# Optimization experiments

Measured on AMD Instinct MI355X. Metric: run time of the kernel, lower is better.

Reference implementation:

```python
import jax, jax.numpy as jnp
import numpy as np

H = 8          # head_num
DK = 16        # qkv_dim
CLIP = 10.0    # logit clipping


def _heads(x):
    # (b, n, H*DK) -> (b, H, n, DK)
    b, n, _ = x.shape
    return x.reshape(b, n, H, DK).transpose(0, 2, 1, 3)


def setup_inputs() -> dict:
    key = jax.random.key(0)
    ks = jax.random.split(key, 10)
    batch, problem, d, klen = 2048, 100, 128, 10
    s = 1.0 / np.sqrt(d)
    problems = jax.random.uniform(ks[0], (batch, problem, 2), dtype=jnp.float32)
    encoded_nodes = jax.random.normal(ks[1], (batch, problem, d), dtype=jnp.float32)
    Wq_first = jax.random.normal(ks[2], (d, H * DK), dtype=jnp.float32) * s
    Wq_last = jax.random.normal(ks[3], (d, H * DK), dtype=jnp.float32) * s
    Wk = jax.random.normal(ks[4], (d, H * DK), dtype=jnp.float32) * s
    Wv = jax.random.normal(ks[5], (d, H * DK), dtype=jnp.float32) * s
    Wcomb = jax.random.normal(ks[6], (H * DK, d), dtype=jnp.float32) * s
    # prefix: k distinct node indices per batch row (first k of a random permutation)
    perm = jax.vmap(lambda kk: jax.random.permutation(kk, problem))(
        jax.random.split(ks[7], batch))
    prefix = perm[:, :klen].astype(jnp.int32)
    return {"problems": problems, "encoded_nodes": encoded_nodes,
            "Wq_first": Wq_first, "Wq_last": Wq_last, "Wk": Wk, "Wv": Wv,
            "Wcomb": Wcomb, "prefix": prefix}


def reference(problems, encoded_nodes, Wq_first, Wq_last, Wk, Wv, Wcomb, prefix):
    batch, problem, d = encoded_nodes.shape
    b_idx = jnp.arange(batch)
    sqrt_dk = jnp.sqrt(jnp.float32(DK))
    sqrt_d = jnp.sqrt(jnp.float32(d))

    # set_kv: precompute multi-head K, V once (single-head key = encoded_nodes)
    kh = _heads(encoded_nodes @ Wk)   # (b, H, n, DK)
    vh = _heads(encoded_nodes @ Wv)   # (b, H, n, DK)

    # set_q1: query contribution of the first node (last node of prefix)
    last0 = prefix[:, -1]
    q1 = _heads(encoded_nodes[b_idx, last0][:, None, :] @ Wq_first)  # (b, H, 1, DK)

    # visited mask from prefix
    visited0 = jnp.zeros((batch, problem), dtype=bool)
    visited0 = visited0.at[b_idx[:, None], prefix].set(True)

    def step(carry, _):
        visited, cur = carry
        enc_last = encoded_nodes[b_idx, cur][:, None, :]            # (b, 1, d)
        q = q1 + _heads(enc_last @ Wq_last)                         # (b, H, 1, DK)
        ninf = jnp.where(visited, -jnp.inf, 0.0)                    # (b, n)
        scores = jnp.einsum('bhqe,bhne->bhqn', q, kh) / sqrt_dk
        att = jax.nn.softmax(scores + ninf[:, None, None, :], axis=-1)
        mh = jnp.einsum('bhqn,bhne->bhqe', att, vh)                 # (b, H, 1, DK)
        mh = mh.transpose(0, 2, 1, 3).reshape(batch, 1, H * DK) @ Wcomb  # (b, 1, d)
        sc = jnp.einsum('bqd,bnd->bqn', mh, encoded_nodes)[:, 0] / sqrt_d  # (b, n)
        logits = CLIP * jnp.tanh(sc) + ninf
        sel = jnp.argmax(logits, axis=-1)                           # (b,)
        visited = visited.at[b_idx, sel].set(True)
        return (visited, sel), sel

    steps = problem - prefix.shape[1]
    _, sels = jax.lax.scan(step, (visited0, last0), None, length=steps)
    tour = jnp.concatenate([prefix, sels.T.astype(prefix.dtype)], axis=1)  # (b, problem)
    return tour
```

## Files before the change

### kernel.cpp

```cpp
#include <hip/hip_runtime.h>
#include <math.h>

#define N      100
#define D      128
#define KL     10
#define S0     90
#define STEPS  90
#define LDK    132
#define NT     512

__device__ __forceinline__ float dot4(float4 a, float4 b) {
  return a.x*b.x + a.y*b.y + a.z*b.z + a.w*b.w;
}
__device__ __forceinline__ void fma4(float4& acc, float a, float4 v) {
  acc.x += a*v.x; acc.y += a*v.y; acc.z += a*v.z; acc.w += a*v.w;
}

template<int RPT>
__device__ __forceinline__ void cc(const float* __restrict__ encB,
                                   const float* __restrict__ W,
                                   bool wRowMajor, int base, int cnt,
                                   const int* __restrict__ slotNode,
                                   float* __restrict__ stage, int tid) {
  const int col = tid & 127;
  const int grp = tid >> 7;
  float acc[RPT];
  int   nd [RPT];
  #pragma unroll
  for (int ii = 0; ii < RPT; ++ii) {
    acc[ii] = 0.f;
    int r = grp + 4*ii;
    nd[ii] = (r < cnt) ? __builtin_amdgcn_readfirstlane(slotNode[base + r]) : 0;
  }
  for (int dd = 0; dd < D; dd += 16) {
    float w[16];
    #pragma unroll
    for (int t = 0; t < 16; ++t)
      w[t] = wRowMajor ? W[col*D + dd + t] : W[(dd+t)*D + col];
    #pragma unroll
    for (int ii = 0; ii < RPT; ++ii) {
      int r = grp + 4*ii;
      if (r < cnt) {
        const float* er = encB + (size_t)nd[ii]*D + dd;
        float a0=0,a1=0,a2=0,a3=0;
        #pragma unroll
        for (int t = 0; t < 16; t += 4) {
          a0 += er[t]*w[t];   a1 += er[t+1]*w[t+1];
          a2 += er[t+2]*w[t+2]; a3 += er[t+3]*w[t+3];
        }
        acc[ii] += (a0+a1)+(a2+a3);
      }
    }
  }
  #pragma unroll
  for (int ii = 0; ii < RPT; ++ii) {
    int r = grp + 4*ii;
    if (r < cnt) stage[(base + r)*LDK + col] = acc[ii];
  }
}

__global__ __launch_bounds__(NT, 4)
void policy_kernel(const float* __restrict__ enc,
                   const float* __restrict__ Wq_first,
                   const float* __restrict__ Wq_last,
                   const float* __restrict__ Wk,
                   const float* __restrict__ Wv,
                   const float* __restrict__ Wcomb,
                   const int*   __restrict__ prefix,
                   int*         __restrict__ out) {
  __shared__ __align__(16) float sCE[S0*LDK];
  __shared__ __align__(16) float sq[D];
  __shared__ __align__(16) float sMh[D];
  __shared__ int   sSlotNode[96];
  __shared__ unsigned long long sPacked[2];
  __shared__ int   sLast0;

  const int tid = threadIdx.x;
  const int b   = blockIdx.x;
  const float* encB = enc + (size_t)b*N*D;

  if (tid < KL) out[(size_t)b*N + tid] = prefix[b*KL + tid];
  if (tid == 0) {
    unsigned vis[4] = {0u,0u,0u,0u};
    const int* pr = prefix + b*KL;
    for (int j = 0; j < KL; ++j) { int n = pr[j]; vis[n>>5] |= 1u << (n&31); }
    int cnt = 0;
    for (int n = 0; n < N; ++n)
      if (!((vis[n>>5] >> (n&31)) & 1u)) sSlotNode[cnt++] = n;
    sLast0 = pr[KL-1];
    sPacked[0] = 0ull; sPacked[1] = 0ull;
  }
  __syncthreads();

  if (tid < D) {
    const int last0 = sLast0;
    const float* er = encB + (size_t)last0*D;
    float a0=0,a1=0,a2=0,a3=0;
    #pragma unroll
    for (int d = 0; d < D; d += 4) {
      a0 += er[d]  *Wq_first[d*D     + tid];
      a1 += er[d+1]*Wq_first[(d+1)*D + tid];
      a2 += er[d+2]*Wq_first[(d+2)*D + tid];
      a3 += er[d+3]*Wq_first[(d+3)*D + tid];
    }
    sMh[tid] = (a0+a1)+(a2+a3);
  }
  __syncthreads();

  const int h = tid >> 6, l = tid & 63;

  {
    const int col = tid & 127;
    const int grp = tid >> 7;
    float acc[23]; int nd[23];
    #pragma unroll
    for (int ii = 0; ii < 23; ++ii) {
      int r = grp + 4*ii;
      acc[ii] = 0.f;
      nd[ii] = (r < S0) ? __builtin_amdgcn_readfirstlane(sSlotNode[r])
                        : ((r == S0) ? sLast0 : 0);
    }
    for (int dd = 0; dd < D; dd += 16) {
      float w[16];
      #pragma unroll
      for (int t = 0; t < 16; ++t) w[t] = Wq_last[(dd+t)*D + col];
      #pragma unroll
      for (int ii = 0; ii < 23; ++ii) {
        int r = grp + 4*ii;
        if (r <= S0) {
          const float* er = encB + (size_t)nd[ii]*D + dd;
          float a0=0,a1=0,a2=0,a3=0;
          #pragma unroll
          for (int t = 0; t < 16; t += 4) {
            a0 += er[t]*w[t];   a1 += er[t+1]*w[t+1];
            a2 += er[t+2]*w[t+2]; a3 += er[t+3]*w[t+3];
          }
          acc[ii] += (a0+a1)+(a2+a3);
        }
      }
    }
    #pragma unroll
    for (int ii = 0; ii < 23; ++ii) {
      int r = grp + 4*ii;
      if (r < S0)       sCE[r*LDK + col] = acc[ii];
      else if (r == S0) sq[col] = acc[ii] + sMh[col];
    }
  }
  __syncthreads();

  const int qcol = (h << 4) | (l & 15);
  const int qrg  = l >> 4;
  float qp[23];
  {
    const float q1c = sMh[qcol];
    #pragma unroll
    for (int ii = 0; ii < 23; ++ii) {
      int r = qrg + 4*ii;
      qp[ii] = (r < S0) ? (sCE[r*LDK + qcol] + q1c) : 0.f;
    }
  }
  __syncthreads();

  cc<23>(encB, Wk, false, 0, S0, sSlotNode, sCE, tid);
  __syncthreads();
  float4 ka0,ka1,ka2,ka3, kb0,kb1,kb2,kb3;
  {
    const float* p = &sCE[l*LDK + h*16];
    ka0 = *(const float4*)(p+0);  ka1 = *(const float4*)(p+4);
    ka2 = *(const float4*)(p+8);  ka3 = *(const float4*)(p+12);
  }
  if (l < 26) {
    const float* p = &sCE[(64+l)*LDK + h*16];
    kb0 = *(const float4*)(p+0);  kb1 = *(const float4*)(p+4);
    kb2 = *(const float4*)(p+8);  kb3 = *(const float4*)(p+12);
  } else {
    kb0=kb1=kb2=kb3 = make_float4(0.f,0.f,0.f,0.f);
  }
  __syncthreads();

  const int cQuad = tid >> 4;
  const int cStrm = tid & 15;
  cc<12>(encB, Wv, false,  0, 48, sSlotNode, sCE, tid);
  cc<12>(encB, Wv, false, 48, 42, sSlotNode, sCE, tid);
  __syncthreads();
  float4 v0,v1,v2,v3,v4,v5;
  v0 = *(const float4*)&sCE[(cStrm     )*LDK + cQuad*4];
  v1 = *(const float4*)&sCE[(cStrm + 16)*LDK + cQuad*4];
  v2 = *(const float4*)&sCE[(cStrm + 32)*LDK + cQuad*4];
  v3 = *(const float4*)&sCE[(cStrm + 48)*LDK + cQuad*4];
  v4 = *(const float4*)&sCE[(cStrm + 64)*LDK + cQuad*4];
  v5 = (cStrm < 10) ? *(const float4*)&sCE[(cStrm + 80)*LDK + cQuad*4]
                    : make_float4(0.f,0.f,0.f,0.f);
  __syncthreads();

  cc<6>(encB, Wcomb, true,  0, 24, sSlotNode, sCE, tid);
  cc<6>(encB, Wcomb, true, 24, 24, sSlotNode, sCE, tid);
  cc<6>(encB, Wcomb, true, 48, 24, sSlotNode, sCE, tid);
  cc<6>(encB, Wcomb, true, 72, 18, sSlotNode, sCE, tid);
  __syncthreads();

  const int di  = tid >> 2;
  const int dkc = tid & 3;
  float visA = 0.f, visB = 0.f, visD = 0.f;

  for (int step = 0; step < STEPS; ++step) {
    float x0, x1;
    {
      const float4 q0 = *(const float4*)&sq[h*16 + 0];
      const float4 q1 = *(const float4*)&sq[h*16 + 4];
      const float4 q2 = *(const float4*)&sq[h*16 + 8];
      const float4 q3 = *(const float4*)&sq[h*16 + 12];
      float s0 = dot4(q0,ka0)+dot4(q1,ka1)+dot4(q2,ka2)+dot4(q3,ka3);
      x0 = expf(s0*0.25f + visA);
      x1 = 0.f;
      if (l < 26) {
        float s1 = dot4(q0,kb0)+dot4(q1,kb1)+dot4(q2,kb2)+dot4(q3,kb3);
        x1 = expf(s1*0.25f + visB);
      }
    }

    {
      const float a0 = __shfl(x0, cStrm);
      const float a1 = __shfl(x0, cStrm + 16);
      const float a2 = __shfl(x0, cStrm + 32);
      const float a3 = __shfl(x0, cStrm + 48);
      const float a4 = __shfl(x1, cStrm);
      const float a5 = __shfl(x1, cStrm + 16);
      float s_loc = (a0+a1)+(a2+a3)+(a4+a5);
      float4 acc = make_float4(0.f,0.f,0.f,0.f);
      fma4(acc, a0, v0);
      fma4(acc, a1, v1);
      fma4(acc, a2, v2);
      fma4(acc, a3, v3);
      fma4(acc, a4, v4);
      fma4(acc, a5, v5);
      #pragma unroll
      for (int off = 1; off < 16; off <<= 1) {
        acc.x += __shfl_xor(acc.x, off);
        acc.y += __shfl_xor(acc.y, off);
        acc.z += __shfl_xor(acc.z, off);
        acc.w += __shfl_xor(acc.w, off);
        s_loc += __shfl_xor(s_loc, off);
      }
      if (cStrm == 0) {
        const float r = 1.0f / s_loc;
        float4 o; o.x=acc.x*r; o.y=acc.y*r; o.z=acc.z*r; o.w=acc.w*r;
        *(float4*)&sMh[((cQuad & 7) << 4) + ((cQuad >> 3) << 2)] = o;
      }
    }
    __syncthreads();

    if (tid == NT-1) sPacked[(step+1)&1] = 0ull;

    if (tid < 384) {
      float a = 0.f;
      #pragma unroll
      for (int j = 0; j < 8; ++j) {
        const float4 ce = *(const float4*)&sCE[di*LDK + dkc*32 + j*4];
        const float4 mh = *(const float4*)&sMh[j*16 + dkc*4];
        a += dot4(ce, mh);
      }
      a += __shfl_xor(a, 1);
      a += __shfl_xor(a, 2);
      float val = (di < S0) ? a + visD : -INFINITY;
      int   idx = (di < S0) ? di : 127;
      #pragma unroll
      for (int off = 4; off <= 32; off <<= 1) {
        float ov = __shfl_xor(val, off);
        int   oi = __shfl_xor(idx, off);
        if (ov > val || (ov == val && oi < idx)) { val = ov; idx = oi; }
      }
      if (l == 0) {
        unsigned s = __float_as_uint(val);
        s = (s & 0x80000000u) ? ~s : (s | 0x80000000u);
        unsigned long long pk = ((unsigned long long)s << 32)
                              | (unsigned long long)(unsigned)(127 - idx);
        atomicMax(&sPacked[step&1], pk);
      }
    }
    __syncthreads();

    {
      const unsigned long long u = sPacked[step & 1];
      const int idx = __builtin_amdgcn_readfirstlane(127 - (int)(u & 0xFFull));
      if (tid == 0) out[(size_t)b*N + KL + step] = sSlotNode[idx];
      if (idx == l)      visA = -INFINITY;
      if (idx == l + 64) visB = -INFINITY;
      if (idx == di)     visD = -INFINITY;
      const int want = idx >> 2;
      float qv = qp[0];
      #pragma unroll
      for (int ii = 1; ii < 23; ++ii) qv = (want == ii) ? qp[ii] : qv;
      if (qrg == (idx & 3)) sq[qcol] = qv;
    }
  }
}

extern "C" void kernel_launch(void* const* d_in, const int* in_sizes, int n_in,
                              void* d_out, int out_size, void* d_ws, size_t ws_size,
                              hipStream_t stream) {
  const float* enc      = (const float*)d_in[1];
  const float* Wq_first = (const float*)d_in[2];
  const float* Wq_last  = (const float*)d_in[3];
  const float* Wk       = (const float*)d_in[4];
  const float* Wv       = (const float*)d_in[5];
  const float* Wcomb    = (const float*)d_in[6];
  const int*   prefix   = (const int*)d_in[7];
  const int batch = in_sizes[7] / KL;
  policy_kernel<<<batch, NT, 0, stream>>>(enc, Wq_first, Wq_last, Wk, Wv, Wcomb,
                                          prefix, (int*)d_out);
}
```

Baseline: 2.280 ms.

## Keep per-node queries in shared memory and hold combined-encoding rows in registers

Moves the Wq_last projection to the end of setup and stores all 91 query rows (bias q1 added) in a shared table. Each step indexes that table by the current node instead of selecting from 23 per-thread registers and writing sq. The Wcomb-projected encoding rows used for the logits are loaded once into 32 registers per thread, so the step loop no longer reads them from shared memory. This trades more register pressure under launch_bounds(512,4) for fewer shared loads and a simpler per-step update.

```diff
diff --git a/kernel.cpp b/kernel.cpp
--- a/kernel.cpp
+++ b/kernel.cpp
@@ -59,6 +59,50 @@
   }
 }
 
+template<int RPT>
+__device__ __forceinline__ void ccq(const float* __restrict__ encB,
+                                    const float* __restrict__ W,
+                                    int base, int cnt,
+                                    const int* __restrict__ slotNode,
+                                    const float* __restrict__ bias,
+                                    float* __restrict__ stage, int tid) {
+  const int col = tid & 127;
+  const int grp = tid >> 7;
+  float acc[RPT];
+  int   nd [RPT];
+  #pragma unroll
+  for (int ii = 0; ii < RPT; ++ii) {
+    acc[ii] = 0.f;
+    int r = grp + 4*ii;
+    nd[ii] = (r < cnt) ? __builtin_amdgcn_readfirstlane(slotNode[base + r]) : 0;
+  }
+  for (int dd = 0; dd < D; dd += 16) {
+    float w[16];
+    #pragma unroll
+    for (int t = 0; t < 16; ++t) w[t] = W[(dd+t)*D + col];
+    #pragma unroll
+    for (int ii = 0; ii < RPT; ++ii) {
+      int r = grp + 4*ii;
+      if (r < cnt) {
+        const float* er = encB + (size_t)nd[ii]*D + dd;
+        float a0=0,a1=0,a2=0,a3=0;
+        #pragma unroll
+        for (int t = 0; t < 16; t += 4) {
+          a0 += er[t]*w[t];   a1 += er[t+1]*w[t+1];
+          a2 += er[t+2]*w[t+2]; a3 += er[t+3]*w[t+3];
+        }
+        acc[ii] += (a0+a1)+(a2+a3);
+      }
+    }
+  }
+  const float bq = bias[col];
+  #pragma unroll
+  for (int ii = 0; ii < RPT; ++ii) {
+    int r = grp + 4*ii;
+    if (r < cnt) stage[(base + r)*LDK + col] = acc[ii] + bq;
+  }
+}
+
 __global__ __launch_bounds__(NT, 4)
 void policy_kernel(const float* __restrict__ enc,
                    const float* __restrict__ Wq_first,
@@ -68,8 +112,7 @@
                    const float* __restrict__ Wcomb,
                    const int*   __restrict__ prefix,
                    int*         __restrict__ out) {
-  __shared__ __align__(16) float sCE[S0*LDK];
-  __shared__ __align__(16) float sq[D];
+  __shared__ __align__(16) float sQ[(S0+1)*LDK];
   __shared__ __align__(16) float sMh[D];
   __shared__ int   sSlotNode[96];
   __shared__ unsigned long long sPacked[2];
@@ -88,6 +131,7 @@
     for (int n = 0; n < N; ++n)
       if (!((vis[n>>5] >> (n&31)) & 1u)) sSlotNode[cnt++] = n;
     sLast0 = pr[KL-1];
+    sSlotNode[S0] = pr[KL-1];
     sPacked[0] = 0ull; sPacked[1] = 0ull;
   }
   __syncthreads();
@@ -109,68 +153,16 @@
 
   const int h = tid >> 6, l = tid & 63;
 
-  {
-    const int col = tid & 127;
-    const int grp = tid >> 7;
-    float acc[23]; int nd[23];
-    #pragma unroll
-    for (int ii = 0; ii < 23; ++ii) {
-      int r = grp + 4*ii;
-      acc[ii] = 0.f;
-      nd[ii] = (r < S0) ? __builtin_amdgcn_readfirstlane(sSlotNode[r])
-                        : ((r == S0) ? sLast0 : 0);
-    }
-    for (int dd = 0; dd < D; dd += 16) {
-      float w[16];
-      #pragma unroll
-      for (int t = 0; t < 16; ++t) w[t] = Wq_last[(dd+t)*D + col];
-      #pragma unroll
-      for (int ii = 0; ii < 23; ++ii) {
-        int r = grp + 4*ii;
-        if (r <= S0) {
-          const float* er = encB + (size_t)nd[ii]*D + dd;
-          float a0=0,a1=0,a2=0,a3=0;
-          #pragma unroll
-          for (int t = 0; t < 16; t += 4) {
-            a0 += er[t]*w[t];   a1 += er[t+1]*w[t+1];
-            a2 += er[t+2]*w[t+2]; a3 += er[t+3]*w[t+3];
-          }
-          acc[ii] += (a0+a1)+(a2+a3);
-        }
-      }
-    }
-    #pragma unroll
-    for (int ii = 0; ii < 23; ++ii) {
-      int r = grp + 4*ii;
-      if (r < S0)       sCE[r*LDK + col] = acc[ii];
-      else if (r == S0) sq[col] = acc[ii] + sMh[col];
-    }
-  }
-  __syncthreads();
-
-  const int qcol = (h << 4) | (l & 15);
-  const int qrg  = l >> 4;
-  float qp[23];
-  {
-    const float q1c = sMh[qcol];
-    #pragma unroll
-    for (int ii = 0; ii < 23; ++ii) {
-      int r = qrg + 4*ii;
-      qp[ii] = (r < S0) ? (sCE[r*LDK + qcol] + q1c) : 0.f;
-    }
-  }
-  __syncthreads();
-
-  cc<23>(encB, Wk, false, 0, S0, sSlotNode, sCE, tid);
+  cc<23>(encB, Wk, false, 0, S0, sSlotNode, sQ, tid);
   __syncthreads();
   float4 ka0,ka1,ka2,ka3, kb0,kb1,kb2,kb3;
   {
-    const float* p = &sCE[l*LDK + h*16];
+    const float* p = &sQ[l*LDK + h*16];
     ka0 = *(const float4*)(p+0);  ka1 = *(const float4*)(p+4);
     ka2 = *(const float4*)(p+8);  ka3 = *(const float4*)(p+12);
   }
   if (l < 26) {
-    const float* p = &sCE[(64+l)*LDK + h*16];
+    const float* p = &sQ[(64+l)*LDK + h*16];
     kb0 = *(const float4*)(p+0);  kb1 = *(const float4*)(p+4);
     kb2 = *(const float4*)(p+8);  kb3 = *(const float4*)(p+12);
   } else {
@@ -180,36 +172,52 @@
 
   const int cQuad = tid >> 4;
   const int cStrm = tid & 15;
-  cc<12>(encB, Wv, false,  0, 48, sSlotNode, sCE, tid);
-  cc<12>(encB, Wv, false, 48, 42, sSlotNode, sCE, tid);
+  cc<12>(encB, Wv, false,  0, 48, sSlotNode, sQ, tid);
+  cc<12>(encB, Wv, false, 48, 42, sSlotNode, sQ, tid);
   __syncthreads();
   float4 v0,v1,v2,v3,v4,v5;
-  v0 = *(const float4*)&sCE[(cStrm     )*LDK + cQuad*4];
-  v1 = *(const float4*)&sCE[(cStrm + 16)*LDK + cQuad*4];
-  v2 = *(const float4*)&sCE[(cStrm + 32)*LDK + cQuad*4];
-  v3 = *(const float4*)&sCE[(cStrm + 48)*LDK + cQuad*4];
-  v4 = *(const float4*)&sCE[(cStrm + 64)*LDK + cQuad*4];
-  v5 = (cStrm < 10) ? *(const float4*)&sCE[(cStrm + 80)*LDK + cQuad*4]
+  v0 = *(const float4*)&sQ[(cStrm     )*LDK + cQuad*4];
+  v1 = *(const float4*)&sQ[(cStrm + 16)*LDK + cQuad*4];
+  v2 = *(const float4*)&sQ[(cStrm + 32)*LDK + cQuad*4];
+  v3 = *(const float4*)&sQ[(cStrm + 48)*LDK + cQuad*4];
+  v4 = *(const float4*)&sQ[(cStrm + 64)*LDK + cQuad*4];
+  v5 = (cStrm < 10) ? *(const float4*)&sQ[(cStrm + 80)*LDK + cQuad*4]
                     : make_float4(0.f,0.f,0.f,0.f);
   __syncthreads();
 
-  cc<6>(encB, Wcomb, true,  0, 24, sSlotNode, sCE, tid);
-  cc<6>(encB, Wcomb, true, 24, 24, sSlotNode, sCE, tid);
-  cc<6>(encB, Wcomb, true, 48, 24, sSlotNode, sCE, tid);
-  cc<6>(encB, Wcomb, true, 72, 18, sSlotNode, sCE, tid);
-  __syncthreads();
-
+  cc<6>(encB, Wcomb, true,  0, 24, sSlotNode, sQ, tid);
+  cc<6>(encB, Wcomb, true, 24, 24, sSlotNode, sQ, tid);
+  cc<6>(encB, Wcomb, true, 48, 24, sSlotNode, sQ, tid);
+  cc<6>(encB, Wcomb, true, 72, 18, sSlotNode, sQ, tid);
+  __syncthreads();
   const int di  = tid >> 2;
   const int dkc = tid & 3;
+  float4 ce[8];
+  if (tid < 384) {
+    #pragma unroll
+    for (int j = 0; j < 8; ++j)
+      ce[j] = *(const float4*)&sQ[di*LDK + dkc*32 + j*4];
+  } else {
+    #pragma unroll
+    for (int j = 0; j < 8; ++j) ce[j] = make_float4(0.f,0.f,0.f,0.f);
+  }
+  __syncthreads();
+
+  ccq<12>(encB, Wq_last,  0, 48, sSlotNode, sMh, sQ, tid);
+  ccq<12>(encB, Wq_last, 48, 43, sSlotNode, sMh, sQ, tid);
+  __syncthreads();
+
+  int   cur  = S0;
   float visA = 0.f, visB = 0.f, visD = 0.f;
 
   for (int step = 0; step < STEPS; ++step) {
     float x0, x1;
     {
-      const float4 q0 = *(const float4*)&sq[h*16 + 0];
-      const float4 q1 = *(const float4*)&sq[h*16 + 4];
-      const float4 q2 = *(const float4*)&sq[h*16 + 8];
-      const float4 q3 = *(const float4*)&sq[h*16 + 12];
+      const float* qr = &sQ[cur*LDK + h*16];
+      const float4 q0 = *(const float4*)(qr + 0);
+      const float4 q1 = *(const float4*)(qr + 4);
+      const float4 q2 = *(const float4*)(qr + 8);
+      const float4 q3 = *(const float4*)(qr + 12);
       float s0 = dot4(q0,ka0)+dot4(q1,ka1)+dot4(q2,ka2)+dot4(q3,ka3);
       x0 = expf(s0*0.25f + visA);
       x1 = 0.f;
@@ -256,9 +264,8 @@
       float a = 0.f;
       #pragma unroll
       for (int j = 0; j < 8; ++j) {
-        const float4 ce = *(const float4*)&sCE[di*LDK + dkc*32 + j*4];
         const float4 mh = *(const float4*)&sMh[j*16 + dkc*4];
-        a += dot4(ce, mh);
+        a += dot4(ce[j], mh);
       }
       a += __shfl_xor(a, 1);
       a += __shfl_xor(a, 2);
@@ -287,11 +294,7 @@
       if (idx == l)      visA = -INFINITY;
       if (idx == l + 64) visB = -INFINITY;
       if (idx == di)     visD = -INFINITY;
-      const int want = idx >> 2;
-      float qv = qp[0];
-      #pragma unroll
-      for (int ii = 1; ii < 23; ++ii) qv = (want == ii) ? qp[ii] : qv;
-      if (qrg == (idx & 3)) sq[qcol] = qv;
+      cur = idx;
     }
   }
 }
```

Result: slower. 3.077 ms (+35.0%).

## Move per-node query table to global workspace to cut registers and raise occupancy

Applied to the files above, without the earlier changes.

The precomputed query rows (q1 plus the Wq_last projection for every candidate node) are now written to a global workspace buffer instead of being held in 23 per-thread registers and broadcast through shared memory each step. Each step reads the selected row straight from global memory by index. This drops the qp register array, the 23-way select chain, a shared buffer and two barriers, and the launch bound is raised from 4 to 6 blocks per SM, with the Wcomb pass split into smaller chunks to lower register pressure. The cost is a dependent global load (likely L2-resident) on the serial step chain and about 93 MB of extra global writes.

```diff
diff --git a/kernel.cpp b/kernel.cpp
--- a/kernel.cpp
+++ b/kernel.cpp
@@ -8,6 +8,9 @@
 #define STEPS  90
 #define LDK    132
 #define NT     512
+#define MAXB   2048
+
+__device__ float g_ws[(size_t)MAXB * (S0+1) * D];
 
 __device__ __forceinline__ float dot4(float4 a, float4 b) {
   return a.x*b.x + a.y*b.y + a.z*b.z + a.w*b.w;
@@ -59,7 +62,7 @@
   }
 }
 
-__global__ __launch_bounds__(NT, 4)
+__global__ __launch_bounds__(NT, 6)
 void policy_kernel(const float* __restrict__ enc,
                    const float* __restrict__ Wq_first,
                    const float* __restrict__ Wq_last,
@@ -67,9 +70,9 @@
                    const float* __restrict__ Wv,
                    const float* __restrict__ Wcomb,
                    const int*   __restrict__ prefix,
+                   float*       __restrict__ wsArg,
                    int*         __restrict__ out) {
   __shared__ __align__(16) float sCE[S0*LDK];
-  __shared__ __align__(16) float sq[D];
   __shared__ __align__(16) float sMh[D];
   __shared__ int   sSlotNode[96];
   __shared__ unsigned long long sPacked[2];
@@ -78,6 +81,7 @@
   const int tid = threadIdx.x;
   const int b   = blockIdx.x;
   const float* encB = enc + (size_t)b*N*D;
+  float* wsQ = (wsArg ? wsArg : g_ws) + (size_t)b*(S0+1)*D;
 
   if (tid < KL) out[(size_t)b*N + tid] = prefix[b*KL + tid];
   if (tid == 0) {
@@ -139,27 +143,13 @@
         }
       }
     }
+    const float q1c = sMh[col];
     #pragma unroll
     for (int ii = 0; ii < 23; ++ii) {
       int r = grp + 4*ii;
-      if (r < S0)       sCE[r*LDK + col] = acc[ii];
-      else if (r == S0) sq[col] = acc[ii] + sMh[col];
-    }
-  }
-  __syncthreads();
-
-  const int qcol = (h << 4) | (l & 15);
-  const int qrg  = l >> 4;
-  float qp[23];
-  {
-    const float q1c = sMh[qcol];
-    #pragma unroll
-    for (int ii = 0; ii < 23; ++ii) {
-      int r = qrg + 4*ii;
-      qp[ii] = (r < S0) ? (sCE[r*LDK + qcol] + q1c) : 0.f;
-    }
-  }
-  __syncthreads();
+      if (r <= S0) wsQ[r*D + col] = acc[ii] + q1c;
+    }
+  }
 
   cc<23>(encB, Wk, false, 0, S0, sSlotNode, sCE, tid);
   __syncthreads();
@@ -193,23 +183,27 @@
                     : make_float4(0.f,0.f,0.f,0.f);
   __syncthreads();
 
-  cc<6>(encB, Wcomb, true,  0, 24, sSlotNode, sCE, tid);
-  cc<6>(encB, Wcomb, true, 24, 24, sSlotNode, sCE, tid);
-  cc<6>(encB, Wcomb, true, 48, 24, sSlotNode, sCE, tid);
-  cc<6>(encB, Wcomb, true, 72, 18, sSlotNode, sCE, tid);
+  cc<4>(encB, Wcomb, true,  0, 16, sSlotNode, sCE, tid);
+  cc<4>(encB, Wcomb, true, 16, 16, sSlotNode, sCE, tid);
+  cc<4>(encB, Wcomb, true, 32, 16, sSlotNode, sCE, tid);
+  cc<4>(encB, Wcomb, true, 48, 16, sSlotNode, sCE, tid);
+  cc<4>(encB, Wcomb, true, 64, 16, sSlotNode, sCE, tid);
+  cc<4>(encB, Wcomb, true, 80, 10, sSlotNode, sCE, tid);
   __syncthreads();
 
   const int di  = tid >> 2;
   const int dkc = tid & 3;
+  int   cur  = S0;
   float visA = 0.f, visB = 0.f, visD = 0.f;
 
   for (int step = 0; step < STEPS; ++step) {
     float x0, x1;
     {
-      const float4 q0 = *(const float4*)&sq[h*16 + 0];
-      const float4 q1 = *(const float4*)&sq[h*16 + 4];
-      const float4 q2 = *(const float4*)&sq[h*16 + 8];
-      const float4 q3 = *(const float4*)&sq[h*16 + 12];
+      const float* qr = wsQ + cur*D + h*16;
+      const float4 q0 = *(const float4*)(qr + 0);
+      const float4 q1 = *(const float4*)(qr + 4);
+      const float4 q2 = *(const float4*)(qr + 8);
+      const float4 q3 = *(const float4*)(qr + 12);
       float s0 = dot4(q0,ka0)+dot4(q1,ka1)+dot4(q2,ka2)+dot4(q3,ka3);
       x0 = expf(s0*0.25f + visA);
       x1 = 0.f;
@@ -287,11 +281,7 @@
       if (idx == l)      visA = -INFINITY;
       if (idx == l + 64) visB = -INFINITY;
       if (idx == di)     visD = -INFINITY;
-      const int want = idx >> 2;
-      float qv = qp[0];
-      #pragma unroll
-      for (int ii = 1; ii < 23; ++ii) qv = (want == ii) ? qp[ii] : qv;
-      if (qrg == (idx & 3)) sq[qcol] = qv;
+      cur = idx;
     }
   }
 }
@@ -307,6 +297,9 @@
   const float* Wcomb    = (const float*)d_in[6];
   const int*   prefix   = (const int*)d_in[7];
   const int batch = in_sizes[7] / KL;
+
+  const size_t need = (size_t)batch * (S0+1) * D * sizeof(float);
+  float* wsq = (d_ws && ws_size >= need) ? (float*)d_ws : nullptr;
   policy_kernel<<<batch, NT, 0, stream>>>(enc, Wq_first, Wq_last, Wk, Wv, Wcomb,
-                                          prefix, (int*)d_out);
-}
+                                          prefix, wsq, (int*)d_out);
+}
```

New measurement: 2.927 ms. 28.4% more time.
